# Optimization experiments

Measured on AMD Instinct MI355X. Metric: run time of the kernel, lower is better.

The kernel has to match this reference:

```python
import jax, jax.numpy as jnp
import numpy as np

FACTOR = 5  # init arg 'factor'


def setup_inputs() -> dict:
    key = jax.random.key(0)
    ks = jax.random.split(key, 9)
    B, L, H, D = 32, 4096, 8, 64
    sh = (B, L, H, D)
    scale = 0.125  # 1/sqrt(D)
    return {
        "queries": jax.random.normal(ks[0], sh, jnp.float32),
        "keys": jax.random.normal(ks[1], sh, jnp.float32),
        "values": jax.random.normal(ks[2], sh, jnp.float32),
        "Wq": jax.random.normal(ks[3], (1, D), jnp.float32) * scale,
        "bq": jax.random.normal(ks[4], (1,), jnp.float32) * scale,
        "Wk": jax.random.normal(ks[5], (1, D), jnp.float32) * scale,
        "bk": jax.random.normal(ks[6], (1,), jnp.float32) * scale,
        "Wv": jax.random.normal(ks[7], (1, D), jnp.float32) * scale,
        "bv": jax.random.normal(ks[8], (1,), jnp.float32) * scale,
    }


def reference(queries, keys, values, Wq, bq, Wk, bk, Wv, bv):
    B, L_Q, H, D = queries.shape
    # transpose(2,1) + LazyLinear(1) + squeeze  ->  scalar series per (b, h, t)
    q = jnp.einsum('blhd,d->bhl', queries, Wq[0]) + bq[0]  # [B,H,L_Q]
    k = jnp.einsum('blhd,d->bhl', keys, Wk[0]) + bk[0]
    v = jnp.einsum('blhd,d->bhl', values, Wv[0]) + bv[0]
    # L_K == L_Q here: torch takes the last L_Q steps (identity in this config)
    k = k[:, :, -L_Q:]
    v = v[:, :, -L_Q:]
    # FFT cross-correlation scores (rfft with n=2L-1 -> L bins; irfft default -> 2L-2)
    n_fft = 2 * L_Q - 1
    Qf = jnp.fft.rfft(q, n_fft)
    Kf = jnp.conj(jnp.fft.rfft(k, n_fft))
    score = jnp.fft.irfft(Qf * Kf)[:, :, :L_Q] / L_Q  # [B,H,L_Q]
    kk = FACTOR * int(np.ceil(np.log(L_Q)))  # 45 for L_Q=4096
    weight, top_idx = jax.lax.top_k(score, kk)  # [B,H,kk]
    weight = jax.nn.softmax(weight, axis=-1)
    # torch: indices = L_Q - top_idx - 1; rolled-V row j is roll(v, j+1),
    # i.e. shift = L_Q - top_idx, so V_sel[b,h,d,t] = v[b,h,(t + top_idx[b,h,d]) % L_Q].
    t = jnp.arange(L_Q)
    gidx = (top_idx[..., None] + t[None, None, None, :]) % L_Q  # [B,H,kk,L_Q]
    V_sel = jnp.take_along_axis(v[:, :, None, :], gidx, axis=-1)  # [B,H,kk,L_Q]
    out = jnp.einsum('bhd,bhdl->bhl', weight, V_sel)  # [B,H,L_Q]
    return out[..., None]  # [B,H,L_Q,1]
```

## Files before the change

kernel.cpp:

```cpp
#include <hip/hip_runtime.h>
#include <math.h>
#include <float.h>

#define L_   4096
#define M_   8192
#define H_   8
#define D_   64
#define KK   45

#define WS_C   0
#define WS_D   4096
#define WS_TW  8192
#define WS_H1  16384
#define WS_H2  24576
#define WS_QKV 32768

__device__ __forceinline__ float2 cadd(float2 a, float2 b) { return make_float2(a.x + b.x, a.y + b.y); }
__device__ __forceinline__ float2 csub(float2 a, float2 b) { return make_float2(a.x - b.x, a.y - b.y); }
__device__ __forceinline__ float2 cmulf(float2 a, float2 b) {
  return make_float2(a.x * b.x - a.y * b.y, a.x * b.y + a.y * b.x);
}
__device__ __forceinline__ float2 cmulcf(float2 a, float2 b) {
  return make_float2(a.x * b.x + a.y * b.y, a.y * b.x - a.x * b.y);
}

template <int NT>
static __device__ void fft_dif(float2* buf, const float2* __restrict__ tw) {
  const int tid = threadIdx.x;
  #pragma unroll
  for (int s = 0; s < 6; ++s) {
    const int q = 2048 >> (2 * s);
    __syncthreads();
    #pragma unroll
    for (int r = 0; r < 2048 / NT; ++r) {
      const int bid = tid + r * NT;
      const int j   = bid & (q - 1);
      const int i0  = ((bid >> (11 - 2 * s)) << (13 - 2 * s)) + j;
      const int e   = j << (2 * s);
      const float2 w1 = tw[e], w2 = tw[2 * e], w3 = tw[3 * e];
      const float2 a = buf[i0], b = buf[i0 + q], c = buf[i0 + 2 * q], d = buf[i0 + 3 * q];
      const float2 t0 = cadd(a, c), t1 = csub(a, c), t2 = cadd(b, d), t3 = csub(b, d);
      buf[i0]         = cadd(t0, t2);
      buf[i0 + q]     = cmulf(make_float2(t1.x + t3.y, t1.y - t3.x), w1);
      buf[i0 + 2 * q] = cmulf(csub(t0, t2), w2);
      buf[i0 + 3 * q] = cmulf(make_float2(t1.x - t3.y, t1.y + t3.x), w3);
    }
  }
  __syncthreads();
  #pragma unroll
  for (int r = 0; r < 4096 / NT; ++r) {
    const int i0 = (tid + r * NT) << 1;
    const float2 a = buf[i0], b = buf[i0 + 1];
    buf[i0] = cadd(a, b); buf[i0 + 1] = csub(a, b);
  }
  __syncthreads();
}

template <int NT>
static __device__ void fft_dit_inv(float2* buf, const float2* __restrict__ tw) {
  const int tid = threadIdx.x;
  __syncthreads();
  #pragma unroll
  for (int r = 0; r < 4096 / NT; ++r) {
    const int i0 = (tid + r * NT) << 1;
    const float2 a = buf[i0], b = buf[i0 + 1];
    buf[i0] = cadd(a, b); buf[i0 + 1] = csub(a, b);
  }
  #pragma unroll
  for (int s = 5; s >= 0; --s) {
    const int q = 2048 >> (2 * s);
    __syncthreads();
    #pragma unroll
    for (int r = 0; r < 2048 / NT; ++r) {
      const int bid = tid + r * NT;
      const int j   = bid & (q - 1);
      const int i0  = ((bid >> (11 - 2 * s)) << (13 - 2 * s)) + j;
      const int e   = j << (2 * s);
      const float2 w1 = tw[e], w2 = tw[2 * e], w3 = tw[3 * e];
      const float2 z0 = buf[i0];
      const float2 z1 = cmulcf(buf[i0 + q],     w1);
      const float2 z2 = cmulcf(buf[i0 + 2 * q], w2);
      const float2 z3 = cmulcf(buf[i0 + 3 * q], w3);
      const float2 t0 = cadd(z0, z2), t1 = csub(z0, z2), t2 = cadd(z1, z3), u = csub(z1, z3);
      buf[i0]         = cadd(t0, t2);
      buf[i0 + q]     = make_float2(t1.x - u.y, t1.y + u.x);
      buf[i0 + 2 * q] = csub(t0, t2);
      buf[i0 + 3 * q] = make_float2(t1.x + u.y, t1.y - u.x);
    }
  }
  __syncthreads();
}

static __device__ void fft_dif2(float2* A, float2* B, const float2* __restrict__ tw) {
  const int tid = threadIdx.x;
  #pragma unroll
  for (int s = 0; s < 6; ++s) {
    const int q = 2048 >> (2 * s);
    __syncthreads();
    #pragma unroll
    for (int r = 0; r < 2; ++r) {
      const int bid = tid + (r << 10);
      const int j   = bid & (q - 1);
      const int i0  = ((bid >> (11 - 2 * s)) << (13 - 2 * s)) + j;
      const int e   = j << (2 * s);
      const float2 w1 = tw[e], w2 = tw[2 * e], w3 = tw[3 * e];
      {
        const float2 a = A[i0], b = A[i0 + q], c = A[i0 + 2 * q], d = A[i0 + 3 * q];
        const float2 t0 = cadd(a, c), t1 = csub(a, c), t2 = cadd(b, d), t3 = csub(b, d);
        A[i0]         = cadd(t0, t2);
        A[i0 + q]     = cmulf(make_float2(t1.x + t3.y, t1.y - t3.x), w1);
        A[i0 + 2 * q] = cmulf(csub(t0, t2), w2);
        A[i0 + 3 * q] = cmulf(make_float2(t1.x - t3.y, t1.y + t3.x), w3);
      }
      {
        const float2 a = B[i0], b = B[i0 + q], c = B[i0 + 2 * q], d = B[i0 + 3 * q];
        const float2 t0 = cadd(a, c), t1 = csub(a, c), t2 = cadd(b, d), t3 = csub(b, d);
        B[i0]         = cadd(t0, t2);
        B[i0 + q]     = cmulf(make_float2(t1.x + t3.y, t1.y - t3.x), w1);
        B[i0 + 2 * q] = cmulf(csub(t0, t2), w2);
        B[i0 + 3 * q] = cmulf(make_float2(t1.x - t3.y, t1.y + t3.x), w3);
      }
    }
  }
  __syncthreads();
  #pragma unroll
  for (int r = 0; r < 4; ++r) {
    const int i0 = (tid + (r << 10)) << 1;
    { const float2 a = A[i0], b = A[i0 + 1]; A[i0] = cadd(a, b); A[i0 + 1] = csub(a, b); }
    { const float2 a = B[i0], b = B[i0 + 1]; B[i0] = cadd(a, b); B[i0 + 1] = csub(a, b); }
  }
  __syncthreads();
}

static __device__ void fft_dit_inv2(float2* A, float2* B, const float2* __restrict__ tw) {
  const int tid = threadIdx.x;
  __syncthreads();
  #pragma unroll
  for (int r = 0; r < 4; ++r) {
    const int i0 = (tid + (r << 10)) << 1;
    { const float2 a = A[i0], b = A[i0 + 1]; A[i0] = cadd(a, b); A[i0 + 1] = csub(a, b); }
    { const float2 a = B[i0], b = B[i0 + 1]; B[i0] = cadd(a, b); B[i0 + 1] = csub(a, b); }
  }
  #pragma unroll
  for (int s = 5; s >= 0; --s) {
    const int q = 2048 >> (2 * s);
    __syncthreads();
    #pragma unroll
    for (int r = 0; r < 2; ++r) {
      const int bid = tid + (r << 10);
      const int j   = bid & (q - 1);
      const int i0  = ((bid >> (11 - 2 * s)) << (13 - 2 * s)) + j;
      const int e   = j << (2 * s);
      const float2 w1 = tw[e], w2 = tw[2 * e], w3 = tw[3 * e];
      {
        const float2 z0 = A[i0];
        const float2 z1 = cmulcf(A[i0 + q], w1);
        const float2 z2 = cmulcf(A[i0 + 2 * q], w2);
        const float2 z3 = cmulcf(A[i0 + 3 * q], w3);
        const float2 t0 = cadd(z0, z2), t1 = csub(z0, z2), t2 = cadd(z1, z3), u = csub(z1, z3);
        A[i0]         = cadd(t0, t2);
        A[i0 + q]     = make_float2(t1.x - u.y, t1.y + u.x);
        A[i0 + 2 * q] = csub(t0, t2);
        A[i0 + 3 * q] = make_float2(t1.x + u.y, t1.y - u.x);
      }
      {
        const float2 z0 = B[i0];
        const float2 z1 = cmulcf(B[i0 + q], w1);
        const float2 z2 = cmulcf(B[i0 + 2 * q], w2);
        const float2 z3 = cmulcf(B[i0 + 3 * q], w3);
        const float2 t0 = cadd(z0, z2), t1 = csub(z0, z2), t2 = cadd(z1, z3), u = csub(z1, z3);
        B[i0]         = cadd(t0, t2);
        B[i0 + q]     = make_float2(t1.x - u.y, t1.y + u.x);
        B[i0 + 2 * q] = csub(t0, t2);
        B[i0 + 3 * q] = make_float2(t1.x + u.y, t1.y - u.x);
      }
    }
  }
  __syncthreads();
}

extern "C" __global__ void setup_tables(float2* ws) {
  const int idx = blockIdx.x * 512 + threadIdx.x;
  if (idx < 4096) {
    const long p = ((long)idx * idx) % 16382;
    const double th = -M_PI * (double)p / 8191.0;
    double s, c; sincos(th, &s, &c);
    ws[WS_C + idx] = make_float2((float)c, (float)s);
  } else if (idx < 8192) {
    const int j = idx - 4096;
    const long p = ((long)j * j) % 16380;
    const double th = M_PI * (double)p / 8190.0;
    double s, c; sincos(th, &s, &c);
    ws[WS_D + j] = make_float2((float)c, (float)s);
  } else if (idx < 16384) {
    const int j = idx - 8192;
    const double th = -M_PI * (double)j / 4096.0;
    double s, c; sincos(th, &s, &c);
    ws[WS_TW + j] = make_float2((float)c, (float)s);
  }
}

extern "C" __global__ __launch_bounds__(512, 1) void setup_filters(float2* ws) {
  __shared__ float2 buf[M_];
  const float2* src = ws + (blockIdx.x == 0 ? WS_C : WS_D);
  float2*       dst = ws + (blockIdx.x == 0 ? WS_H1 : WS_H2);
  const float2* tw  = ws + WS_TW;
  for (int i = threadIdx.x; i < M_; i += 512) {
    float2 val = make_float2(0.f, 0.f);
    if (i != 4096) {
      const int jj = (i <= 4095) ? i : (M_ - i);
      const float2 e = src[jj];
      val = make_float2(e.x, -e.y);
    }
    buf[i] = val;
  }
  fft_dif<512>(buf, tw);
  const float sc = 1.0f / 8192.0f;
  for (int i = threadIdx.x; i < M_; i += 512)
    dst[i] = make_float2(buf[i].x * sc, buf[i].y * sc);
}

extern "C" __global__ __launch_bounds__(256)
void proj_kernel(const float* __restrict__ queries, const float* __restrict__ keys,
                 const float* __restrict__ values,
                 const float* __restrict__ Wq, const float* __restrict__ bq,
                 const float* __restrict__ Wk, const float* __restrict__ bk,
                 const float* __restrict__ Wv, const float* __restrict__ bv,
                 float* __restrict__ q_ws, float* __restrict__ k_ws,
                 float* __restrict__ v_ws)
{
  const int tid   = threadIdx.x;
  const int wave  = tid >> 6;
  const int lane  = tid & 63;
  const int lane16 = lane & 15;
  const int hq    = lane >> 4;
  const int blk   = blockIdx.x;
  const int b     = blk >> 6;
  const int lbase = (blk & 63) << 6;

  const float* srcs[3] = {queries, keys, values};
  const float* Wsx[3]  = {Wq, Wk, Wv};
  const float* Bsx[3]  = {bq, bk, bv};
  float* dsts[3] = {q_ws, k_ws, v_ws};

  #pragma unroll
  for (int s = 0; s < 3; ++s) {
    const float* base = srcs[s] + (size_t)b * (L_ * 512);
    const float4 w4 = reinterpret_cast<const float4*>(Wsx[s])[lane16];
    const float bias = Bsx[s][0];
    float* dst = dsts[s];
    for (int ii = 0; ii < 4; ++ii) {
      float4 xa[4], xb[4];
      #pragma unroll
      for (int u = 0; u < 4; ++u) {
        const int l = lbase + (((ii << 2) + u) << 2) + wave;
        const float4* p = reinterpret_cast<const float4*>(base + (size_t)l * 512);
        xa[u] = p[lane];
        xb[u] = p[64 + lane];
      }
      #pragma unroll
      for (int u = 0; u < 4; ++u) {
        const int l = lbase + (((ii << 2) + u) << 2) + wave;
        if (s < 2) {
          double d1 = (double)xa[u].x * w4.x + (double)xa[u].y * w4.y +
                      (double)xa[u].z * w4.z + (double)xa[u].w * w4.w;
          double d2 = (double)xb[u].x * w4.x + (double)xb[u].y * w4.y +
                      (double)xb[u].z * w4.z + (double)xb[u].w * w4.w;
          d1 += __shfl_xor(d1, 1); d2 += __shfl_xor(d2, 1);
          d1 += __shfl_xor(d1, 2); d2 += __shfl_xor(d2, 2);
          d1 += __shfl_xor(d1, 4); d2 += __shfl_xor(d2, 4);
          d1 += __shfl_xor(d1, 8); d2 += __shfl_xor(d2, 8);
          if (lane16 == 0) {
            dst[((size_t)(b * 8 + hq)     << 12) + l] = (float)(d1 + (double)bias);
            dst[((size_t)(b * 8 + hq + 4) << 12) + l] = (float)(d2 + (double)bias);
          }
        } else {
          float f1 = xa[u].x * w4.x + xa[u].y * w4.y + xa[u].z * w4.z + xa[u].w * w4.w;
          float f2 = xb[u].x * w4.x + xb[u].y * w4.y + xb[u].z * w4.z + xb[u].w * w4.w;
          f1 += __shfl_xor(f1, 1); f2 += __shfl_xor(f2, 1);
          f1 += __shfl_xor(f1, 2); f2 += __shfl_xor(f2, 2);
          f1 += __shfl_xor(f1, 4); f2 += __shfl_xor(f2, 4);
          f1 += __shfl_xor(f1, 8); f2 += __shfl_xor(f2, 8);
          if (lane16 == 0) {
            dst[((size_t)(b * 8 + hq)     << 12) + l] = f1 + bias;
            dst[((size_t)(b * 8 + hq + 4) << 12) + l] = f2 + bias;
          }
        }
      }
    }
  }
}

extern "C" __global__ __launch_bounds__(1024, 1)
void autocorr_main(const float2* __restrict__ ws,
                   const float* __restrict__ q_ws, const float* __restrict__ k_ws,
                   const float* __restrict__ v_ws, float* __restrict__ outp)
{
  __shared__ float2 bufA[M_];
  __shared__ float2 bufB[M_];
  __shared__ float  v_lds[L_];
  __shared__ float  cand_v[16 * KK];
  __shared__ int    cand_i[16 * KK];
  __shared__ float  w_sh[KK];
  __shared__ int    i_sh[KK];

  const int tid = threadIdx.x;
  const int bh  = blockIdx.x;

  const float2* c_t = ws + WS_C;
  const float2* d_t = ws + WS_D;
  const float2* tw  = ws + WS_TW;
  const float2* H1  = ws + WS_H1;
  const float2* H2  = ws + WS_H2;
  const float* qrow = q_ws + ((size_t)bh << 12);
  const float* krow = k_ws + ((size_t)bh << 12);
  const float* vrow = v_ws + ((size_t)bh << 12);

  #pragma unroll
  for (int r = 0; r < 4; ++r) {
    const int i = tid + (r << 10);
    v_lds[i] = vrow[i];
    const float2 cc = c_t[i];
    const float kv = krow[i];
    const float qv = qrow[i];
    bufA[i] = make_float2(kv * cc.x, kv * cc.y);
    bufB[i] = make_float2(qv * cc.x, qv * cc.y);
  }
  #pragma unroll
  for (int r = 4; r < 8; ++r) {
    const int i = tid + (r << 10);
    bufA[i] = make_float2(0.f, 0.f);
    bufB[i] = make_float2(0.f, 0.f);
  }

  fft_dif2(bufA, bufB, tw);
  #pragma unroll
  for (int r = 0; r < 8; ++r) {
    const int i = tid + (r << 10);
    bufA[i] = cmulf(bufA[i], H1[i]);
    bufB[i] = cmulf(bufB[i], H1[i]);
  }
  fft_dit_inv2(bufA, bufB, tw);

  #pragma unroll
  for (int r = 0; r < 4; ++r) {
    const int m = tid + (r << 10);
    const float2 cc = c_t[m];
    const float2 K = cmulf(cc, bufA[m]);
    const float2 Q = cmulf(cc, bufB[m]);
    const float2 F = cmulcf(Q, K);
    float2 g;
    if (m == 0 || m == 4095) g = make_float2(F.x, 0.f);
    else                     g = make_float2(2.f * F.x, 2.f * F.y);
    bufA[m] = cmulf(g, d_t[m]);
  }
  #pragma unroll
  for (int r = 4; r < 8; ++r) bufA[tid + (r << 10)] = make_float2(0.f, 0.f);

  fft_dif<1024>(bufA, tw);
  #pragma unroll
  for (int r = 0; r < 8; ++r) {
    const int i = tid + (r << 10);
    bufA[i] = cmulf(bufA[i], H2[i]);
  }
  fft_dit_inv<1024>(bufA, tw);

  const float SCALE = (float)(1.0 / (8190.0 * 4096.0));
  float svv[4]; int sii[4];
  #pragma unroll
  for (int r = 0; r < 4; ++r) {
    const int t = tid + (r << 10);
    const float2 Z = cmulf(d_t[t], bufA[t]);
    svv[r] = Z.x * SCALE;
    sii[r] = t;
  }
  const int lane = tid & 63, wv = tid >> 6;
  for (int it = 0; it < KK; ++it) {
    float bvv = -FLT_MAX; int bii = 0x7fffffff;
    #pragma unroll
    for (int c = 0; c < 4; ++c)
      if (svv[c] > bvv || (svv[c] == bvv && sii[c] < bii)) { bvv = svv[c]; bii = sii[c]; }
    #pragma unroll
    for (int off = 1; off < 64; off <<= 1) {
      const float ov = __shfl_xor(bvv, off);
      const int   oi = __shfl_xor(bii, off);
      if (ov > bvv || (ov == bvv && oi < bii)) { bvv = ov; bii = oi; }
    }
    #pragma unroll
    for (int c = 0; c < 4; ++c) if (sii[c] == bii) svv[c] = -FLT_MAX;
    if (lane == 0) { cand_v[wv * KK + it] = bvv; cand_i[wv * KK + it] = bii; }
  }
  __syncthreads();

  if (tid < 64) {
    float mv[12]; int mi[12];
    #pragma unroll
    for (int c = 0; c < 12; ++c) {
      const int id = tid + 64 * c;
      if (id < 16 * KK) { mv[c] = cand_v[id]; mi[c] = cand_i[id]; }
      else              { mv[c] = -FLT_MAX;   mi[c] = 0x7fffffff; }
    }
    float m0 = 0.f, sum = 0.f, myv = -FLT_MAX; int myi = 0;
    for (int it = 0; it < KK; ++it) {
      float bvv = -FLT_MAX; int bii = 0x7fffffff;
      #pragma unroll
      for (int c = 0; c < 12; ++c)
        if (mv[c] > bvv || (mv[c] == bvv && mi[c] < bii)) { bvv = mv[c]; bii = mi[c]; }
      #pragma unroll
      for (int off = 1; off < 64; off <<= 1) {
        const float ov = __shfl_xor(bvv, off);
        const int   oi = __shfl_xor(bii, off);
        if (ov > bvv || (ov == bvv && oi < bii)) { bvv = ov; bii = oi; }
      }
      if (it == 0) m0 = bvv;
      sum += expf(bvv - m0);
      if (tid == it) { myv = bvv; myi = bii; }
      #pragma unroll
      for (int c = 0; c < 12; ++c) if (mi[c] == bii) mv[c] = -FLT_MAX;
    }
    if (tid < KK) { w_sh[tid] = expf(myv - m0) / sum; i_sh[tid] = myi; }
  }
  __syncthreads();

  {
    float acc[4] = {0, 0, 0, 0};
    for (int j = 0; j < KK; ++j) {
      const float wj = w_sh[j];
      const int   bse = i_sh[j] + tid;
      #pragma unroll
      for (int r = 0; r < 4; ++r)
        acc[r] = fmaf(wj, v_lds[(bse + (r << 10)) & (L_ - 1)], acc[r]);
    }
    float* op = outp + ((size_t)bh << 12);
    #pragma unroll
    for (int r = 0; r < 4; ++r) op[tid + (r << 10)] = acc[r];
  }
}

extern "C" void kernel_launch(void* const* d_in, const int* in_sizes, int n_in,
                              void* d_out, int out_size, void* d_ws, size_t ws_size,
                              hipStream_t stream) {
  const float* queries = (const float*)d_in[0];
  const float* keys    = (const float*)d_in[1];
  const float* values  = (const float*)d_in[2];
  const float* Wq = (const float*)d_in[3];
  const float* bq = (const float*)d_in[4];
  const float* Wk = (const float*)d_in[5];
  const float* bk = (const float*)d_in[6];
  const float* Wv = (const float*)d_in[7];
  const float* bv = (const float*)d_in[8];
  float2* ws = (float2*)d_ws;
  float* q_ws = (float*)d_ws + 2 * WS_QKV;
  float* k_ws = q_ws + (1 << 20);
  float* v_ws = k_ws + (1 << 20);
  float* out = (float*)d_out;

  hipLaunchKernelGGL(setup_tables,  dim3(32), dim3(512), 0, stream, ws);
  hipLaunchKernelGGL(setup_filters, dim3(2),  dim3(512), 0, stream, ws);
  hipLaunchKernelGGL(proj_kernel,   dim3(2048), dim3(256), 0, stream,
                     queries, keys, values, Wq, bq, Wk, bk, Wv, bv, q_ws, k_ws, v_ws);
  hipLaunchKernelGGL(autocorr_main, dim3(256), dim3(1024), 0, stream,
                     ws, q_ws, k_ws, v_ws, out);
}
```

Before: 344.1 us.

## Fuse input projections into autocorrelation kernel, overlapping loads with FFT stages

Removes the separate projection kernel and its global q/k/v scratch round-trip. The K projection is now computed inside the main kernel. The Q and V projections are prefetched in chunks and reduced through hooks placed between FFT stages, so global loads overlap the LDS-bound FFT work. The two batched FFTs become sequential single FFTs, and the q/k dot products drop from double to float accumulation. This risks lower memory-level parallelism, since only 256 blocks now stream all the input, and slightly different top-k selection.

```diff
diff --git a/kernel.cpp b/kernel.cpp
--- a/kernel.cpp
+++ b/kernel.cpp
@@ -13,7 +13,6 @@
 #define WS_TW  8192
 #define WS_H1  16384
 #define WS_H2  24576
-#define WS_QKV 32768
 
 __device__ __forceinline__ float2 cadd(float2 a, float2 b) { return make_float2(a.x + b.x, a.y + b.y); }
 __device__ __forceinline__ float2 csub(float2 a, float2 b) { return make_float2(a.x - b.x, a.y - b.y); }
@@ -24,13 +23,14 @@
   return make_float2(a.x * b.x + a.y * b.y, a.y * b.x - a.x * b.y);
 }
 
-template <int NT>
-static __device__ void fft_dif(float2* buf, const float2* __restrict__ tw) {
+template <int NT, typename F>
+static __device__ void fft_dif_h(float2* buf, const float2* __restrict__ tw, F&& hook) {
   const int tid = threadIdx.x;
   #pragma unroll
   for (int s = 0; s < 6; ++s) {
     const int q = 2048 >> (2 * s);
     __syncthreads();
+    hook();
     #pragma unroll
     for (int r = 0; r < 2048 / NT; ++r) {
       const int bid = tid + r * NT;
@@ -47,6 +47,7 @@
     }
   }
   __syncthreads();
+  hook();
   #pragma unroll
   for (int r = 0; r < 4096 / NT; ++r) {
     const int i0 = (tid + r * NT) << 1;
@@ -56,10 +57,11 @@
   __syncthreads();
 }
 
-template <int NT>
-static __device__ void fft_dit_inv(float2* buf, const float2* __restrict__ tw) {
+template <int NT, typename F>
+static __device__ void fft_dit_inv_h(float2* buf, const float2* __restrict__ tw, F&& hook) {
   const int tid = threadIdx.x;
   __syncthreads();
+  hook();
   #pragma unroll
   for (int r = 0; r < 4096 / NT; ++r) {
     const int i0 = (tid + r * NT) << 1;
@@ -70,6 +72,7 @@
   for (int s = 5; s >= 0; --s) {
     const int q = 2048 >> (2 * s);
     __syncthreads();
+    hook();
     #pragma unroll
     for (int r = 0; r < 2048 / NT; ++r) {
       const int bid = tid + r * NT;
@@ -86,94 +89,6 @@
       buf[i0 + q]     = make_float2(t1.x - u.y, t1.y + u.x);
       buf[i0 + 2 * q] = csub(t0, t2);
       buf[i0 + 3 * q] = make_float2(t1.x + u.y, t1.y - u.x);
-    }
-  }
-  __syncthreads();
-}
-
-static __device__ void fft_dif2(float2* A, float2* B, const float2* __restrict__ tw) {
-  const int tid = threadIdx.x;
-  #pragma unroll
-  for (int s = 0; s < 6; ++s) {
-    const int q = 2048 >> (2 * s);
-    __syncthreads();
-    #pragma unroll
-    for (int r = 0; r < 2; ++r) {
-      const int bid = tid + (r << 10);
-      const int j   = bid & (q - 1);
-      const int i0  = ((bid >> (11 - 2 * s)) << (13 - 2 * s)) + j;
-      const int e   = j << (2 * s);
-      const float2 w1 = tw[e], w2 = tw[2 * e], w3 = tw[3 * e];
-      {
-        const float2 a = A[i0], b = A[i0 + q], c = A[i0 + 2 * q], d = A[i0 + 3 * q];
-        const float2 t0 = cadd(a, c), t1 = csub(a, c), t2 = cadd(b, d), t3 = csub(b, d);
-        A[i0]         = cadd(t0, t2);
-        A[i0 + q]     = cmulf(make_float2(t1.x + t3.y, t1.y - t3.x), w1);
-        A[i0 + 2 * q] = cmulf(csub(t0, t2), w2);
-        A[i0 + 3 * q] = cmulf(make_float2(t1.x - t3.y, t1.y + t3.x), w3);
-      }
-      {
-        const float2 a = B[i0], b = B[i0 + q], c = B[i0 + 2 * q], d = B[i0 + 3 * q];
-        const float2 t0 = cadd(a, c), t1 = csub(a, c), t2 = cadd(b, d), t3 = csub(b, d);
-        B[i0]         = cadd(t0, t2);
-        B[i0 + q]     = cmulf(make_float2(t1.x + t3.y, t1.y - t3.x), w1);
-        B[i0 + 2 * q] = cmulf(csub(t0, t2), w2);
-        B[i0 + 3 * q] = cmulf(make_float2(t1.x - t3.y, t1.y + t3.x), w3);
-      }
-    }
-  }
-  __syncthreads();
-  #pragma unroll
-  for (int r = 0; r < 4; ++r) {
-    const int i0 = (tid + (r << 10)) << 1;
-    { const float2 a = A[i0], b = A[i0 + 1]; A[i0] = cadd(a, b); A[i0 + 1] = csub(a, b); }
-    { const float2 a = B[i0], b = B[i0 + 1]; B[i0] = cadd(a, b); B[i0 + 1] = csub(a, b); }
-  }
-  __syncthreads();
-}
-
-static __device__ void fft_dit_inv2(float2* A, float2* B, const float2* __restrict__ tw) {
-  const int tid = threadIdx.x;
-  __syncthreads();
-  #pragma unroll
-  for (int r = 0; r < 4; ++r) {
-    const int i0 = (tid + (r << 10)) << 1;
-    { const float2 a = A[i0], b = A[i0 + 1]; A[i0] = cadd(a, b); A[i0 + 1] = csub(a, b); }
-    { const float2 a = B[i0], b = B[i0 + 1]; B[i0] = cadd(a, b); B[i0 + 1] = csub(a, b); }
-  }
-  #pragma unroll
-  for (int s = 5; s >= 0; --s) {
-    const int q = 2048 >> (2 * s);
-    __syncthreads();
-    #pragma unroll
-    for (int r = 0; r < 2; ++r) {
-      const int bid = tid + (r << 10);
-      const int j   = bid & (q - 1);
-      const int i0  = ((bid >> (11 - 2 * s)) << (13 - 2 * s)) + j;
-      const int e   = j << (2 * s);
-      const float2 w1 = tw[e], w2 = tw[2 * e], w3 = tw[3 * e];
-      {
-        const float2 z0 = A[i0];
-        const float2 z1 = cmulcf(A[i0 + q], w1);
-        const float2 z2 = cmulcf(A[i0 + 2 * q], w2);
-        const float2 z3 = cmulcf(A[i0 + 3 * q], w3);
-        const float2 t0 = cadd(z0, z2), t1 = csub(z0, z2), t2 = cadd(z1, z3), u = csub(z1, z3);
-        A[i0]         = cadd(t0, t2);
-        A[i0 + q]     = make_float2(t1.x - u.y, t1.y + u.x);
-        A[i0 + 2 * q] = csub(t0, t2);
-        A[i0 + 3 * q] = make_float2(t1.x + u.y, t1.y - u.x);
-      }
-      {
-        const float2 z0 = B[i0];
-        const float2 z1 = cmulcf(B[i0 + q], w1);
-        const float2 z2 = cmulcf(B[i0 + 2 * q], w2);
-        const float2 z3 = cmulcf(B[i0 + 3 * q], w3);
-        const float2 t0 = cadd(z0, z2), t1 = csub(z0, z2), t2 = cadd(z1, z3), u = csub(z1, z3);
-        B[i0]         = cadd(t0, t2);
-        B[i0 + q]     = make_float2(t1.x - u.y, t1.y + u.x);
-        B[i0 + 2 * q] = csub(t0, t2);
-        B[i0 + 3 * q] = make_float2(t1.x + u.y, t1.y - u.x);
-      }
     }
   }
   __syncthreads();
@@ -214,87 +129,19 @@
     }
     buf[i] = val;
   }
-  fft_dif<512>(buf, tw);
+  fft_dif_h<512>(buf, tw, [] __device__ () {});
   const float sc = 1.0f / 8192.0f;
   for (int i = threadIdx.x; i < M_; i += 512)
     dst[i] = make_float2(buf[i].x * sc, buf[i].y * sc);
 }
 
-extern "C" __global__ __launch_bounds__(256)
-void proj_kernel(const float* __restrict__ queries, const float* __restrict__ keys,
-                 const float* __restrict__ values,
-                 const float* __restrict__ Wq, const float* __restrict__ bq,
-                 const float* __restrict__ Wk, const float* __restrict__ bk,
-                 const float* __restrict__ Wv, const float* __restrict__ bv,
-                 float* __restrict__ q_ws, float* __restrict__ k_ws,
-                 float* __restrict__ v_ws)
-{
-  const int tid   = threadIdx.x;
-  const int wave  = tid >> 6;
-  const int lane  = tid & 63;
-  const int lane16 = lane & 15;
-  const int hq    = lane >> 4;
-  const int blk   = blockIdx.x;
-  const int b     = blk >> 6;
-  const int lbase = (blk & 63) << 6;
-
-  const float* srcs[3] = {queries, keys, values};
-  const float* Wsx[3]  = {Wq, Wk, Wv};
-  const float* Bsx[3]  = {bq, bk, bv};
-  float* dsts[3] = {q_ws, k_ws, v_ws};
-
-  #pragma unroll
-  for (int s = 0; s < 3; ++s) {
-    const float* base = srcs[s] + (size_t)b * (L_ * 512);
-    const float4 w4 = reinterpret_cast<const float4*>(Wsx[s])[lane16];
-    const float bias = Bsx[s][0];
-    float* dst = dsts[s];
-    for (int ii = 0; ii < 4; ++ii) {
-      float4 xa[4], xb[4];
-      #pragma unroll
-      for (int u = 0; u < 4; ++u) {
-        const int l = lbase + (((ii << 2) + u) << 2) + wave;
-        const float4* p = reinterpret_cast<const float4*>(base + (size_t)l * 512);
-        xa[u] = p[lane];
-        xb[u] = p[64 + lane];
-      }
-      #pragma unroll
-      for (int u = 0; u < 4; ++u) {
-        const int l = lbase + (((ii << 2) + u) << 2) + wave;
-        if (s < 2) {
-          double d1 = (double)xa[u].x * w4.x + (double)xa[u].y * w4.y +
-                      (double)xa[u].z * w4.z + (double)xa[u].w * w4.w;
-          double d2 = (double)xb[u].x * w4.x + (double)xb[u].y * w4.y +
-                      (double)xb[u].z * w4.z + (double)xb[u].w * w4.w;
-          d1 += __shfl_xor(d1, 1); d2 += __shfl_xor(d2, 1);
-          d1 += __shfl_xor(d1, 2); d2 += __shfl_xor(d2, 2);
-          d1 += __shfl_xor(d1, 4); d2 += __shfl_xor(d2, 4);
-          d1 += __shfl_xor(d1, 8); d2 += __shfl_xor(d2, 8);
-          if (lane16 == 0) {
-            dst[((size_t)(b * 8 + hq)     << 12) + l] = (float)(d1 + (double)bias);
-            dst[((size_t)(b * 8 + hq + 4) << 12) + l] = (float)(d2 + (double)bias);
-          }
-        } else {
-          float f1 = xa[u].x * w4.x + xa[u].y * w4.y + xa[u].z * w4.z + xa[u].w * w4.w;
-          float f2 = xb[u].x * w4.x + xb[u].y * w4.y + xb[u].z * w4.z + xb[u].w * w4.w;
-          f1 += __shfl_xor(f1, 1); f2 += __shfl_xor(f2, 1);
-          f1 += __shfl_xor(f1, 2); f2 += __shfl_xor(f2, 2);
-          f1 += __shfl_xor(f1, 4); f2 += __shfl_xor(f2, 4);
-          f1 += __shfl_xor(f1, 8); f2 += __shfl_xor(f2, 8);
-          if (lane16 == 0) {
-            dst[((size_t)(b * 8 + hq)     << 12) + l] = f1 + bias;
-            dst[((size_t)(b * 8 + hq + 4) << 12) + l] = f2 + bias;
-          }
-        }
-      }
-    }
-  }
-}
-
-extern "C" __global__ __launch_bounds__(1024, 1)
-void autocorr_main(const float2* __restrict__ ws,
-                   const float* __restrict__ q_ws, const float* __restrict__ k_ws,
-                   const float* __restrict__ v_ws, float* __restrict__ outp)
+extern "C" __global__ __launch_bounds__(1024, 4)
+void autocorr_fused(const float* __restrict__ queries, const float* __restrict__ keys,
+                    const float* __restrict__ values,
+                    const float* __restrict__ Wq, const float* __restrict__ bq,
+                    const float* __restrict__ Wk, const float* __restrict__ bk,
+                    const float* __restrict__ Wv, const float* __restrict__ bv,
+                    const float2* __restrict__ ws, float* __restrict__ outp)
 {
   __shared__ float2 bufA[M_];
   __shared__ float2 bufB[M_];
@@ -306,49 +153,153 @@
 
   const int tid = threadIdx.x;
   const int bh  = blockIdx.x;
+  const int b   = bh >> 3;
+  const int h   = bh & 7;
+  const int lane16 = tid & 15;
+  const int grp    = tid >> 4;
 
   const float2* c_t = ws + WS_C;
   const float2* d_t = ws + WS_D;
   const float2* tw  = ws + WS_TW;
   const float2* H1  = ws + WS_H1;
   const float2* H2  = ws + WS_H2;
-  const float* qrow = q_ws + ((size_t)bh << 12);
-  const float* krow = k_ws + ((size_t)bh << 12);
-  const float* vrow = v_ws + ((size_t)bh << 12);
-
+
+  const size_t rowoff = ((size_t)b * L_ * H_ + h) * (size_t)D_;
+  const float* Xq = queries + rowoff;
+  const float* Xk = keys    + rowoff;
+  const float* Xv = values  + rowoff;
+  const float4 w4q = reinterpret_cast<const float4*>(Wq)[lane16];
+  const float4 w4k = reinterpret_cast<const float4*>(Wk)[lane16];
+  const float4 w4v = reinterpret_cast<const float4*>(Wv)[lane16];
+  const float bq0 = bq[0], bk0 = bk[0], bv0 = bv[0];
+
+  float* kst = reinterpret_cast<float*>(bufA) + 8192;
+  float* qst = reinterpret_cast<float*>(bufB) + 8192;
+
+  {
+    float4 KA[8], KB[8];
+    #pragma unroll
+    for (int u = 0; u < 8; ++u)
+      KA[u] = reinterpret_cast<const float4*>(Xk + (size_t)((u << 6) + grp) * 512)[lane16];
+    #pragma unroll
+    for (int q4 = 0; q4 < 4; ++q4) {
+      const int base = q4 * 16;
+      #pragma unroll
+      for (int u = 0; u < 8; ++u)
+        KB[u] = reinterpret_cast<const float4*>(Xk + (size_t)(((base + 8 + u) << 6) + grp) * 512)[lane16];
+      #pragma unroll
+      for (int u = 0; u < 8; ++u) {
+        float vv = KA[u].x * w4k.x + KA[u].y * w4k.y + KA[u].z * w4k.z + KA[u].w * w4k.w;
+        vv += __shfl_xor(vv, 1); vv += __shfl_xor(vv, 2);
+        vv += __shfl_xor(vv, 4); vv += __shfl_xor(vv, 8);
+        if (lane16 == 0) kst[((base + u) << 6) + grp] = vv + bk0;
+      }
+      if (q4 < 3) {
+        #pragma unroll
+        for (int u = 0; u < 8; ++u)
+          KA[u] = reinterpret_cast<const float4*>(Xk + (size_t)(((base + 16 + u) << 6) + grp) * 512)[lane16];
+      }
+      #pragma unroll
+      for (int u = 0; u < 8; ++u) {
+        float vv = KB[u].x * w4k.x + KB[u].y * w4k.y + KB[u].z * w4k.z + KB[u].w * w4k.w;
+        vv += __shfl_xor(vv, 1); vv += __shfl_xor(vv, 2);
+        vv += __shfl_xor(vv, 4); vv += __shfl_xor(vv, 8);
+        if (lane16 == 0) kst[((base + 8 + u) << 6) + grp] = vv + bk0;
+      }
+    }
+  }
+  __syncthreads();
+  float kv[4];
+  #pragma unroll
+  for (int r = 0; r < 4; ++r) kv[r] = kst[tid + (r << 10)];
+  __syncthreads();
   #pragma unroll
   for (int r = 0; r < 4; ++r) {
     const int i = tid + (r << 10);
-    v_lds[i] = vrow[i];
     const float2 cc = c_t[i];
-    const float kv = krow[i];
-    const float qv = qrow[i];
-    bufA[i] = make_float2(kv * cc.x, kv * cc.y);
-    bufB[i] = make_float2(qv * cc.x, qv * cc.y);
-  }
-  #pragma unroll
-  for (int r = 4; r < 8; ++r) {
+    bufA[i] = make_float2(kv[r] * cc.x, kv[r] * cc.y);
+  }
+  #pragma unroll
+  for (int r = 4; r < 8; ++r) bufA[tid + (r << 10)] = make_float2(0.f, 0.f);
+
+  int cq = 0;
+  float4 pfq[4];
+  auto issueQ = [&](int cb) {
+    #pragma unroll
+    for (int u = 0; u < 4; ++u)
+      pfq[u] = reinterpret_cast<const float4*>(Xq + (size_t)(((cb + u) << 6) + grp) * 512)[lane16];
+  };
+  auto hookQ = [&]() {
+    #pragma unroll
+    for (int u = 0; u < 4; ++u) {
+      float vv = pfq[u].x * w4q.x + pfq[u].y * w4q.y + pfq[u].z * w4q.z + pfq[u].w * w4q.w;
+      vv += __shfl_xor(vv, 1); vv += __shfl_xor(vv, 2);
+      vv += __shfl_xor(vv, 4); vv += __shfl_xor(vv, 8);
+      if (lane16 == 0) qst[((cq + u) << 6) + grp] = vv + bq0;
+    }
+    cq += 4;
+    if (cq < 64) issueQ(cq);
+  };
+  issueQ(0);
+
+  fft_dif_h<1024>(bufA, tw, hookQ);
+  hookQ();
+  #pragma unroll
+  for (int r = 0; r < 8; ++r) { const int i = tid + (r << 10); bufA[i] = cmulf(bufA[i], H1[i]); }
+  fft_dit_inv_h<1024>(bufA, tw, hookQ);
+  hookQ();
+
+  float2 Kr[4];
+  #pragma unroll
+  for (int r = 0; r < 4; ++r) { const int m = tid + (r << 10); Kr[r] = cmulf(c_t[m], bufA[m]); }
+
+  __syncthreads();
+  float qv[4];
+  #pragma unroll
+  for (int r = 0; r < 4; ++r) qv[r] = qst[tid + (r << 10)];
+  __syncthreads();
+  #pragma unroll
+  for (int r = 0; r < 4; ++r) {
     const int i = tid + (r << 10);
-    bufA[i] = make_float2(0.f, 0.f);
-    bufB[i] = make_float2(0.f, 0.f);
-  }
-
-  fft_dif2(bufA, bufB, tw);
-  #pragma unroll
-  for (int r = 0; r < 8; ++r) {
-    const int i = tid + (r << 10);
-    bufA[i] = cmulf(bufA[i], H1[i]);
-    bufB[i] = cmulf(bufB[i], H1[i]);
-  }
-  fft_dit_inv2(bufA, bufB, tw);
+    const float2 cc = c_t[i];
+    bufB[i] = make_float2(qv[r] * cc.x, qv[r] * cc.y);
+  }
+  #pragma unroll
+  for (int r = 4; r < 8; ++r) bufB[tid + (r << 10)] = make_float2(0.f, 0.f);
+
+  int cv = 0;
+  float4 pfv[4];
+  auto issueV = [&](int cb) {
+    #pragma unroll
+    for (int u = 0; u < 4; ++u)
+      pfv[u] = reinterpret_cast<const float4*>(Xv + (size_t)(((cb + u) << 6) + grp) * 512)[lane16];
+  };
+  auto hookV = [&]() {
+    #pragma unroll
+    for (int u = 0; u < 4; ++u) {
+      float vv = pfv[u].x * w4v.x + pfv[u].y * w4v.y + pfv[u].z * w4v.z + pfv[u].w * w4v.w;
+      vv += __shfl_xor(vv, 1); vv += __shfl_xor(vv, 2);
+      vv += __shfl_xor(vv, 4); vv += __shfl_xor(vv, 8);
+      if (lane16 == 0) v_lds[((cv + u) << 6) + grp] = vv + bv0;
+    }
+    cv += 4;
+    if (cv < 64) issueV(cv);
+  };
+  issueV(0);
+
+  fft_dif_h<1024>(bufB, tw, hookV);
+  hookV();
+  #pragma unroll
+  for (int r = 0; r < 8; ++r) { const int i = tid + (r << 10); bufB[i] = cmulf(bufB[i], H1[i]); }
+  fft_dit_inv_h<1024>(bufB, tw, hookV);
+  hookV();
 
   #pragma unroll
   for (int r = 0; r < 4; ++r) {
     const int m = tid + (r << 10);
     const float2 cc = c_t[m];
-    const float2 K = cmulf(cc, bufA[m]);
     const float2 Q = cmulf(cc, bufB[m]);
-    const float2 F = cmulcf(Q, K);
+    const float2 F = cmulcf(Q, Kr[r]);
     float2 g;
     if (m == 0 || m == 4095) g = make_float2(F.x, 0.f);
     else                     g = make_float2(2.f * F.x, 2.f * F.y);
@@ -357,13 +308,11 @@
   #pragma unroll
   for (int r = 4; r < 8; ++r) bufA[tid + (r << 10)] = make_float2(0.f, 0.f);
 
-  fft_dif<1024>(bufA, tw);
-  #pragma unroll
-  for (int r = 0; r < 8; ++r) {
-    const int i = tid + (r << 10);
-    bufA[i] = cmulf(bufA[i], H2[i]);
-  }
-  fft_dit_inv<1024>(bufA, tw);
+  auto noh = [] __device__ () {};
+  fft_dif_h<1024>(bufA, tw, noh);
+  #pragma unroll
+  for (int r = 0; r < 8; ++r) { const int i = tid + (r << 10); bufA[i] = cmulf(bufA[i], H2[i]); }
+  fft_dit_inv_h<1024>(bufA, tw, noh);
 
   const float SCALE = (float)(1.0 / (8190.0 * 4096.0));
   float svv[4]; int sii[4];
@@ -450,15 +399,10 @@
   const float* Wv = (const float*)d_in[7];
   const float* bv = (const float*)d_in[8];
   float2* ws = (float2*)d_ws;
-  float* q_ws = (float*)d_ws + 2 * WS_QKV;
-  float* k_ws = q_ws + (1 << 20);
-  float* v_ws = k_ws + (1 << 20);
   float* out = (float*)d_out;
 
   hipLaunchKernelGGL(setup_tables,  dim3(32), dim3(512), 0, stream, ws);
   hipLaunchKernelGGL(setup_filters, dim3(2),  dim3(512), 0, stream, ws);
-  hipLaunchKernelGGL(proj_kernel,   dim3(2048), dim3(256), 0, stream,
-                     queries, keys, values, Wq, bq, Wk, bk, Wv, bv, q_ws, k_ws, v_ws);
-  hipLaunchKernelGGL(autocorr_main, dim3(256), dim3(1024), 0, stream,
-                     ws, q_ws, k_ws, v_ws, out);
-}
+  hipLaunchKernelGGL(autocorr_fused, dim3(256), dim3(1024), 0, stream,
+                     queries, keys, values, Wq, bq, Wk, bk, Wv, bv, ws, out);
+}
```

Measured after the change: 366.9 us. 1.07x slower.

## Fuse radix-2 stages with filter multiply, compute twiddles on the fly, restructure projection

Applied to the files above, without the earlier changes.

The Bluestein convolutions are restructured so the final DIF radix-2 stage, the spectral filter multiply and the first DIT radix-2 stage run as one vectorized float4 pass. This removes two barriers and two LDS round-trips per convolution. Twiddles are now computed with __sincosf plus complex products instead of being read from a global table, trading memory loads for ALU work at some cost in accuracy. The q/k projection also drops its double-precision accumulation, uses a four-lane shuffle reduction with per-lane 64-element loads, and the main kernel's initial loads are vectorized.

```diff
diff --git a/kernel.cpp b/kernel.cpp
--- a/kernel.cpp
+++ b/kernel.cpp
@@ -24,157 +24,144 @@
   return make_float2(a.x * b.x + a.y * b.y, a.y * b.x - a.x * b.y);
 }
 
-template <int NT>
-static __device__ void fft_dif(float2* buf, const float2* __restrict__ tw) {
+__device__ __forceinline__ float2 twf(int e) {
+  float s, c;
+  __sincosf((float)e * -7.66990394e-4f, &s, &c);
+  return make_float2(c, s);
+}
+
+#define R4DIF(BUF) { \
+  const float2 a = BUF[i0], b = BUF[i0 + q], c = BUF[i0 + 2 * q], d = BUF[i0 + 3 * q]; \
+  const float2 t0 = cadd(a, c), t1 = csub(a, c), t2 = cadd(b, d), t3 = csub(b, d); \
+  BUF[i0]         = cadd(t0, t2); \
+  BUF[i0 + q]     = cmulf(make_float2(t1.x + t3.y, t1.y - t3.x), w1); \
+  BUF[i0 + 2 * q] = cmulf(csub(t0, t2), w2); \
+  BUF[i0 + 3 * q] = cmulf(make_float2(t1.x - t3.y, t1.y + t3.x), w3); }
+
+#define R4DIT(BUF) { \
+  const float2 z0 = BUF[i0]; \
+  const float2 z1 = cmulcf(BUF[i0 + q],     w1); \
+  const float2 z2 = cmulcf(BUF[i0 + 2 * q], w2); \
+  const float2 z3 = cmulcf(BUF[i0 + 3 * q], w3); \
+  const float2 t0 = cadd(z0, z2), t1 = csub(z0, z2), t2 = cadd(z1, z3), u = csub(z1, z3); \
+  BUF[i0]         = cadd(t0, t2); \
+  BUF[i0 + q]     = make_float2(t1.x - u.y, t1.y + u.x); \
+  BUF[i0 + 2 * q] = csub(t0, t2); \
+  BUF[i0 + 3 * q] = make_float2(t1.x + u.y, t1.y - u.x); }
+
+__device__ __forceinline__ float4 midpair(float4 a, float4 h) {
+  float2 u = make_float2(a.x + a.z, a.y + a.w);
+  float2 v = make_float2(a.x - a.z, a.y - a.w);
+  u = cmulf(u, make_float2(h.x, h.y));
+  v = cmulf(v, make_float2(h.z, h.w));
+  return make_float4(u.x + v.x, u.y + v.y, u.x - v.x, u.y - v.y);
+}
+
+static __device__ void conv2(float2* A, float2* B, const float2* __restrict__ Hf) {
   const int tid = threadIdx.x;
   #pragma unroll
   for (int s = 0; s < 6; ++s) {
     const int q = 2048 >> (2 * s);
     __syncthreads();
     #pragma unroll
+    for (int r = 0; r < 2; ++r) {
+      const int bid = tid + (r << 10);
+      const int j   = bid & (q - 1);
+      const int i0  = ((bid >> (11 - 2 * s)) << (13 - 2 * s)) + j;
+      const float2 w1 = twf(j << (2 * s));
+      const float2 w2 = cmulf(w1, w1);
+      const float2 w3 = cmulf(w2, w1);
+      R4DIF(A) R4DIF(B)
+    }
+  }
+  __syncthreads();
+  #pragma unroll
+  for (int r = 0; r < 4; ++r) {
+    const int p = tid + (r << 10);
+    const float4 h = reinterpret_cast<const float4*>(Hf)[p];
+    reinterpret_cast<float4*>(A)[p] = midpair(reinterpret_cast<float4*>(A)[p], h);
+    reinterpret_cast<float4*>(B)[p] = midpair(reinterpret_cast<float4*>(B)[p], h);
+  }
+  #pragma unroll
+  for (int s = 5; s >= 0; --s) {
+    const int q = 2048 >> (2 * s);
+    __syncthreads();
+    #pragma unroll
+    for (int r = 0; r < 2; ++r) {
+      const int bid = tid + (r << 10);
+      const int j   = bid & (q - 1);
+      const int i0  = ((bid >> (11 - 2 * s)) << (13 - 2 * s)) + j;
+      const float2 w1 = twf(j << (2 * s));
+      const float2 w2 = cmulf(w1, w1);
+      const float2 w3 = cmulf(w2, w1);
+      R4DIT(A) R4DIT(B)
+    }
+  }
+  __syncthreads();
+}
+
+static __device__ void conv1(float2* A, const float2* __restrict__ Hf) {
+  const int tid = threadIdx.x;
+  #pragma unroll
+  for (int s = 0; s < 6; ++s) {
+    const int q = 2048 >> (2 * s);
+    __syncthreads();
+    #pragma unroll
+    for (int r = 0; r < 2; ++r) {
+      const int bid = tid + (r << 10);
+      const int j   = bid & (q - 1);
+      const int i0  = ((bid >> (11 - 2 * s)) << (13 - 2 * s)) + j;
+      const float2 w1 = twf(j << (2 * s));
+      const float2 w2 = cmulf(w1, w1);
+      const float2 w3 = cmulf(w2, w1);
+      R4DIF(A)
+    }
+  }
+  __syncthreads();
+  #pragma unroll
+  for (int r = 0; r < 4; ++r) {
+    const int p = tid + (r << 10);
+    const float4 h = reinterpret_cast<const float4*>(Hf)[p];
+    reinterpret_cast<float4*>(A)[p] = midpair(reinterpret_cast<float4*>(A)[p], h);
+  }
+  #pragma unroll
+  for (int s = 5; s >= 0; --s) {
+    const int q = 2048 >> (2 * s);
+    __syncthreads();
+    #pragma unroll
+    for (int r = 0; r < 2; ++r) {
+      const int bid = tid + (r << 10);
+      const int j   = bid & (q - 1);
+      const int i0  = ((bid >> (11 - 2 * s)) << (13 - 2 * s)) + j;
+      const float2 w1 = twf(j << (2 * s));
+      const float2 w2 = cmulf(w1, w1);
+      const float2 w3 = cmulf(w2, w1);
+      R4DIT(A)
+    }
+  }
+  __syncthreads();
+}
+
+template <int NT>
+static __device__ void fft_dif_tab(float2* buf, const float2* __restrict__ tw) {
+  const int tid = threadIdx.x;
+  for (int s = 0; s < 6; ++s) {
+    const int q = 2048 >> (2 * s);
+    __syncthreads();
     for (int r = 0; r < 2048 / NT; ++r) {
       const int bid = tid + r * NT;
       const int j   = bid & (q - 1);
       const int i0  = ((bid >> (11 - 2 * s)) << (13 - 2 * s)) + j;
       const int e   = j << (2 * s);
       const float2 w1 = tw[e], w2 = tw[2 * e], w3 = tw[3 * e];
-      const float2 a = buf[i0], b = buf[i0 + q], c = buf[i0 + 2 * q], d = buf[i0 + 3 * q];
-      const float2 t0 = cadd(a, c), t1 = csub(a, c), t2 = cadd(b, d), t3 = csub(b, d);
-      buf[i0]         = cadd(t0, t2);
-      buf[i0 + q]     = cmulf(make_float2(t1.x + t3.y, t1.y - t3.x), w1);
-      buf[i0 + 2 * q] = cmulf(csub(t0, t2), w2);
-      buf[i0 + 3 * q] = cmulf(make_float2(t1.x - t3.y, t1.y + t3.x), w3);
-    }
-  }
-  __syncthreads();
-  #pragma unroll
+      R4DIF(buf)
+    }
+  }
+  __syncthreads();
   for (int r = 0; r < 4096 / NT; ++r) {
     const int i0 = (tid + r * NT) << 1;
     const float2 a = buf[i0], b = buf[i0 + 1];
     buf[i0] = cadd(a, b); buf[i0 + 1] = csub(a, b);
-  }
-  __syncthreads();
-}
-
-template <int NT>
-static __device__ void fft_dit_inv(float2* buf, const float2* __restrict__ tw) {
-  const int tid = threadIdx.x;
-  __syncthreads();
-  #pragma unroll
-  for (int r = 0; r < 4096 / NT; ++r) {
-    const int i0 = (tid + r * NT) << 1;
-    const float2 a = buf[i0], b = buf[i0 + 1];
-    buf[i0] = cadd(a, b); buf[i0 + 1] = csub(a, b);
-  }
-  #pragma unroll
-  for (int s = 5; s >= 0; --s) {
-    const int q = 2048 >> (2 * s);
-    __syncthreads();
-    #pragma unroll
-    for (int r = 0; r < 2048 / NT; ++r) {
-      const int bid = tid + r * NT;
-      const int j   = bid & (q - 1);
-      const int i0  = ((bid >> (11 - 2 * s)) << (13 - 2 * s)) + j;
-      const int e   = j << (2 * s);
-      const float2 w1 = tw[e], w2 = tw[2 * e], w3 = tw[3 * e];
-      const float2 z0 = buf[i0];
-      const float2 z1 = cmulcf(buf[i0 + q],     w1);
-      const float2 z2 = cmulcf(buf[i0 + 2 * q], w2);
-      const float2 z3 = cmulcf(buf[i0 + 3 * q], w3);
-      const float2 t0 = cadd(z0, z2), t1 = csub(z0, z2), t2 = cadd(z1, z3), u = csub(z1, z3);
-      buf[i0]         = cadd(t0, t2);
-      buf[i0 + q]     = make_float2(t1.x - u.y, t1.y + u.x);
-      buf[i0 + 2 * q] = csub(t0, t2);
-      buf[i0 + 3 * q] = make_float2(t1.x + u.y, t1.y - u.x);
-    }
-  }
-  __syncthreads();
-}
-
-static __device__ void fft_dif2(float2* A, float2* B, const float2* __restrict__ tw) {
-  const int tid = threadIdx.x;
-  #pragma unroll
-  for (int s = 0; s < 6; ++s) {
-    const int q = 2048 >> (2 * s);
-    __syncthreads();
-    #pragma unroll
-    for (int r = 0; r < 2; ++r) {
-      const int bid = tid + (r << 10);
-      const int j   = bid & (q - 1);
-      const int i0  = ((bid >> (11 - 2 * s)) << (13 - 2 * s)) + j;
-      const int e   = j << (2 * s);
-      const float2 w1 = tw[e], w2 = tw[2 * e], w3 = tw[3 * e];
-      {
-        const float2 a = A[i0], b = A[i0 + q], c = A[i0 + 2 * q], d = A[i0 + 3 * q];
-        const float2 t0 = cadd(a, c), t1 = csub(a, c), t2 = cadd(b, d), t3 = csub(b, d);
-        A[i0]         = cadd(t0, t2);
-        A[i0 + q]     = cmulf(make_float2(t1.x + t3.y, t1.y - t3.x), w1);
-        A[i0 + 2 * q] = cmulf(csub(t0, t2), w2);
-        A[i0 + 3 * q] = cmulf(make_float2(t1.x - t3.y, t1.y + t3.x), w3);
-      }
-      {
-        const float2 a = B[i0], b = B[i0 + q], c = B[i0 + 2 * q], d = B[i0 + 3 * q];
-        const float2 t0 = cadd(a, c), t1 = csub(a, c), t2 = cadd(b, d), t3 = csub(b, d);
-        B[i0]         = cadd(t0, t2);
-        B[i0 + q]     = cmulf(make_float2(t1.x + t3.y, t1.y - t3.x), w1);
-        B[i0 + 2 * q] = cmulf(csub(t0, t2), w2);
-        B[i0 + 3 * q] = cmulf(make_float2(t1.x - t3.y, t1.y + t3.x), w3);
-      }
-    }
-  }
-  __syncthreads();
-  #pragma unroll
-  for (int r = 0; r < 4; ++r) {
-    const int i0 = (tid + (r << 10)) << 1;
-    { const float2 a = A[i0], b = A[i0 + 1]; A[i0] = cadd(a, b); A[i0 + 1] = csub(a, b); }
-    { const float2 a = B[i0], b = B[i0 + 1]; B[i0] = cadd(a, b); B[i0 + 1] = csub(a, b); }
-  }
-  __syncthreads();
-}
-
-static __device__ void fft_dit_inv2(float2* A, float2* B, const float2* __restrict__ tw) {
-  const int tid = threadIdx.x;
-  __syncthreads();
-  #pragma unroll
-  for (int r = 0; r < 4; ++r) {
-    const int i0 = (tid + (r << 10)) << 1;
-    { const float2 a = A[i0], b = A[i0 + 1]; A[i0] = cadd(a, b); A[i0 + 1] = csub(a, b); }
-    { const float2 a = B[i0], b = B[i0 + 1]; B[i0] = cadd(a, b); B[i0 + 1] = csub(a, b); }
-  }
-  #pragma unroll
-  for (int s = 5; s >= 0; --s) {
-    const int q = 2048 >> (2 * s);
-    __syncthreads();
-    #pragma unroll
-    for (int r = 0; r < 2; ++r) {
-      const int bid = tid + (r << 10);
-      const int j   = bid & (q - 1);
-      const int i0  = ((bid >> (11 - 2 * s)) << (13 - 2 * s)) + j;
-      const int e   = j << (2 * s);
-      const float2 w1 = tw[e], w2 = tw[2 * e], w3 = tw[3 * e];
-      {
-        const float2 z0 = A[i0];
-        const float2 z1 = cmulcf(A[i0 + q], w1);
-        const float2 z2 = cmulcf(A[i0 + 2 * q], w2);
-        const float2 z3 = cmulcf(A[i0 + 3 * q], w3);
-        const float2 t0 = cadd(z0, z2), t1 = csub(z0, z2), t2 = cadd(z1, z3), u = csub(z1, z3);
-        A[i0]         = cadd(t0, t2);
-        A[i0 + q]     = make_float2(t1.x - u.y, t1.y + u.x);
-        A[i0 + 2 * q] = csub(t0, t2);
-        A[i0 + 3 * q] = make_float2(t1.x + u.y, t1.y - u.x);
-      }
-      {
-        const float2 z0 = B[i0];
-        const float2 z1 = cmulcf(B[i0 + q], w1);
-        const float2 z2 = cmulcf(B[i0 + 2 * q], w2);
-        const float2 z3 = cmulcf(B[i0 + 3 * q], w3);
-        const float2 t0 = cadd(z0, z2), t1 = csub(z0, z2), t2 = cadd(z1, z3), u = csub(z1, z3);
-        B[i0]         = cadd(t0, t2);
-        B[i0 + q]     = make_float2(t1.x - u.y, t1.y + u.x);
-        B[i0 + 2 * q] = csub(t0, t2);
-        B[i0 + 3 * q] = make_float2(t1.x + u.y, t1.y - u.x);
-      }
-    }
   }
   __syncthreads();
 }
@@ -201,7 +188,7 @@
 }
 
 extern "C" __global__ __launch_bounds__(512, 1) void setup_filters(float2* ws) {
-  __shared__ float2 buf[M_];
+  __shared__ __align__(16) float2 buf[M_];
   const float2* src = ws + (blockIdx.x == 0 ? WS_C : WS_D);
   float2*       dst = ws + (blockIdx.x == 0 ? WS_H1 : WS_H2);
   const float2* tw  = ws + WS_TW;
@@ -214,7 +201,7 @@
     }
     buf[i] = val;
   }
-  fft_dif<512>(buf, tw);
+  fft_dif_tab<512>(buf, tw);
   const float sc = 1.0f / 8192.0f;
   for (int i = threadIdx.x; i < M_; i += 512)
     dst[i] = make_float2(buf[i].x * sc, buf[i].y * sc);
@@ -229,13 +216,15 @@
                  float* __restrict__ q_ws, float* __restrict__ k_ws,
                  float* __restrict__ v_ws)
 {
-  const int tid   = threadIdx.x;
-  const int wave  = tid >> 6;
-  const int lane  = tid & 63;
-  const int lane16 = lane & 15;
-  const int hq    = lane >> 4;
-  const int blk   = blockIdx.x;
-  const int b     = blk >> 6;
+  const int tid  = threadIdx.x;
+  const int wave = tid >> 6;
+  const int lane = tid & 63;
+  const int qt   = lane & 3;
+  const int rr   = lane >> 2;
+  const int hh   = rr & 7;
+  const int dl   = rr >> 3;
+  const int blk  = blockIdx.x;
+  const int b    = blk >> 6;
   const int lbase = (blk & 63) << 6;
 
   const float* srcs[3] = {queries, keys, values};
@@ -245,47 +234,36 @@
 
   #pragma unroll
   for (int s = 0; s < 3; ++s) {
-    const float* base = srcs[s] + (size_t)b * (L_ * 512);
-    const float4 w4 = reinterpret_cast<const float4*>(Wsx[s])[lane16];
+    const float4* src4 = reinterpret_cast<const float4*>(srcs[s]) + (size_t)b * 524288;
+    const float4* W4   = reinterpret_cast<const float4*>(Wsx[s]);
+    float4 w[4];
+    #pragma unroll
+    for (int j = 0; j < 4; ++j) w[j] = W4[qt * 4 + j];
     const float bias = Bsx[s][0];
-    float* dst = dsts[s];
-    for (int ii = 0; ii < 4; ++ii) {
+    float* dst = dsts[s] + ((size_t)(b * 8 + hh) << 12);
+
+    #pragma unroll
+    for (int st = 0; st < 4; ++st) {
+      const int l0a = lbase + st * 16 + wave * 2;
+      const int l0b = l0a + 8;
+      const float4* pa = src4 + (size_t)l0a * 128 + lane * 4;
+      const float4* pb = src4 + (size_t)l0b * 128 + lane * 4;
       float4 xa[4], xb[4];
       #pragma unroll
-      for (int u = 0; u < 4; ++u) {
-        const int l = lbase + (((ii << 2) + u) << 2) + wave;
-        const float4* p = reinterpret_cast<const float4*>(base + (size_t)l * 512);
-        xa[u] = p[lane];
-        xb[u] = p[64 + lane];
+      for (int j = 0; j < 4; ++j) xa[j] = pa[j];
+      #pragma unroll
+      for (int j = 0; j < 4; ++j) xb[j] = pb[j];
+      float fa = 0.f, fb = 0.f;
+      #pragma unroll
+      for (int j = 0; j < 4; ++j) {
+        fa += xa[j].x * w[j].x + xa[j].y * w[j].y + xa[j].z * w[j].z + xa[j].w * w[j].w;
+        fb += xb[j].x * w[j].x + xb[j].y * w[j].y + xb[j].z * w[j].z + xb[j].w * w[j].w;
       }
-      #pragma unroll
-      for (int u = 0; u < 4; ++u) {
-        const int l = lbase + (((ii << 2) + u) << 2) + wave;
-        if (s < 2) {
-          double d1 = (double)xa[u].x * w4.x + (double)xa[u].y * w4.y +
-                      (double)xa[u].z * w4.z + (double)xa[u].w * w4.w;
-          double d2 = (double)xb[u].x * w4.x + (double)xb[u].y * w4.y +
-                      (double)xb[u].z * w4.z + (double)xb[u].w * w4.w;
-          d1 += __shfl_xor(d1, 1); d2 += __shfl_xor(d2, 1);
-          d1 += __shfl_xor(d1, 2); d2 += __shfl_xor(d2, 2);
-          d1 += __shfl_xor(d1, 4); d2 += __shfl_xor(d2, 4);
-          d1 += __shfl_xor(d1, 8); d2 += __shfl_xor(d2, 8);
-          if (lane16 == 0) {
-            dst[((size_t)(b * 8 + hq)     << 12) + l] = (float)(d1 + (double)bias);
-            dst[((size_t)(b * 8 + hq + 4) << 12) + l] = (float)(d2 + (double)bias);
-          }
-        } else {
-          float f1 = xa[u].x * w4.x + xa[u].y * w4.y + xa[u].z * w4.z + xa[u].w * w4.w;
-          float f2 = xb[u].x * w4.x + xb[u].y * w4.y + xb[u].z * w4.z + xb[u].w * w4.w;
-          f1 += __shfl_xor(f1, 1); f2 += __shfl_xor(f2, 1);
-          f1 += __shfl_xor(f1, 2); f2 += __shfl_xor(f2, 2);
-          f1 += __shfl_xor(f1, 4); f2 += __shfl_xor(f2, 4);
-          f1 += __shfl_xor(f1, 8); f2 += __shfl_xor(f2, 8);
-          if (lane16 == 0) {
-            dst[((size_t)(b * 8 + hq)     << 12) + l] = f1 + bias;
-            dst[((size_t)(b * 8 + hq + 4) << 12) + l] = f2 + bias;
-          }
-        }
+      fa += __shfl_xor(fa, 1); fb += __shfl_xor(fb, 1);
+      fa += __shfl_xor(fa, 2); fb += __shfl_xor(fb, 2);
+      if (qt == 0) {
+        dst[l0a + dl] = fa + bias;
+        dst[l0b + dl] = fb + bias;
       }
     }
   }
@@ -296,8 +274,8 @@
                    const float* __restrict__ q_ws, const float* __restrict__ k_ws,
                    const float* __restrict__ v_ws, float* __restrict__ outp)
 {
-  __shared__ float2 bufA[M_];
-  __shared__ float2 bufB[M_];
+  __shared__ __align__(16) float2 bufA[M_];
+  __shared__ __align__(16) float2 bufB[M_];
   __shared__ float  v_lds[L_];
   __shared__ float  cand_v[16 * KK];
   __shared__ int    cand_i[16 * KK];
@@ -309,38 +287,31 @@
 
   const float2* c_t = ws + WS_C;
   const float2* d_t = ws + WS_D;
-  const float2* tw  = ws + WS_TW;
   const float2* H1  = ws + WS_H1;
   const float2* H2  = ws + WS_H2;
   const float* qrow = q_ws + ((size_t)bh << 12);
   const float* krow = k_ws + ((size_t)bh << 12);
   const float* vrow = v_ws + ((size_t)bh << 12);
 
-  #pragma unroll
-  for (int r = 0; r < 4; ++r) {
-    const int i = tid + (r << 10);
-    v_lds[i] = vrow[i];
-    const float2 cc = c_t[i];
-    const float kv = krow[i];
-    const float qv = qrow[i];
-    bufA[i] = make_float2(kv * cc.x, kv * cc.y);
-    bufB[i] = make_float2(qv * cc.x, qv * cc.y);
-  }
-  #pragma unroll
-  for (int r = 4; r < 8; ++r) {
-    const int i = tid + (r << 10);
-    bufA[i] = make_float2(0.f, 0.f);
-    bufB[i] = make_float2(0.f, 0.f);
-  }
-
-  fft_dif2(bufA, bufB, tw);
-  #pragma unroll
-  for (int r = 0; r < 8; ++r) {
-    const int i = tid + (r << 10);
-    bufA[i] = cmulf(bufA[i], H1[i]);
-    bufB[i] = cmulf(bufB[i], H1[i]);
-  }
-  fft_dit_inv2(bufA, bufB, tw);
+  {
+    const float4 v4 = reinterpret_cast<const float4*>(vrow)[tid];
+    reinterpret_cast<float4*>(v_lds)[tid] = v4;
+    const float4 k4 = reinterpret_cast<const float4*>(krow)[tid];
+    const float4 q4 = reinterpret_cast<const float4*>(qrow)[tid];
+    const float4 c01 = reinterpret_cast<const float4*>(c_t)[2 * tid];
+    const float4 c23 = reinterpret_cast<const float4*>(c_t)[2 * tid + 1];
+    float4* A4 = reinterpret_cast<float4*>(bufA);
+    float4* B4 = reinterpret_cast<float4*>(bufB);
+    A4[2 * tid]     = make_float4(k4.x * c01.x, k4.x * c01.y, k4.y * c01.z, k4.y * c01.w);
+    A4[2 * tid + 1] = make_float4(k4.z * c23.x, k4.z * c23.y, k4.w * c23.z, k4.w * c23.w);
+    B4[2 * tid]     = make_float4(q4.x * c01.x, q4.x * c01.y, q4.y * c01.z, q4.y * c01.w);
+    B4[2 * tid + 1] = make_float4(q4.z * c23.x, q4.z * c23.y, q4.w * c23.z, q4.w * c23.w);
+    const float4 z = make_float4(0.f, 0.f, 0.f, 0.f);
+    A4[2048 + tid] = z; A4[3072 + tid] = z;
+    B4[2048 + tid] = z; B4[3072 + tid] = z;
+  }
+
+  conv2(bufA, bufB, H1);
 
   #pragma unroll
   for (int r = 0; r < 4; ++r) {
@@ -357,13 +328,7 @@
   #pragma unroll
   for (int r = 4; r < 8; ++r) bufA[tid + (r << 10)] = make_float2(0.f, 0.f);
 
-  fft_dif<1024>(bufA, tw);
-  #pragma unroll
-  for (int r = 0; r < 8; ++r) {
-    const int i = tid + (r << 10);
-    bufA[i] = cmulf(bufA[i], H2[i]);
-  }
-  fft_dit_inv<1024>(bufA, tw);
+  conv1(bufA, H2);
 
   const float SCALE = (float)(1.0 / (8190.0 * 4096.0));
   float svv[4]; int sii[4];
```

Result: no change. 340.0 us (-1.2%).
